# Kernel optimization log

Hardware: AMD Instinct MI355X
Metric: run time of the kernel (lower is better)

The kernel has to match this reference:

```python
import jax, jax.numpy as jnp
import numpy as np

K = 20
BN_EPS = 1e-5
NEG_SLOPE = 0.2


def knn_idx(x, k):
    # x: [B, C, N]; returns indices of k nearest neighbors per point: [B, N, k]
    sq = jnp.sum(x * x, axis=1)                      # [B, N]
    inner = jnp.einsum('bcn,bcm->bnm', x, x)         # [B, N, N]
    dist = sq[:, :, None] + sq[:, None, :] - 2.0 * inner  # squared distances
    _, idx = jax.lax.top_k(-dist, k)                 # smallest distances
    return idx


def get_graph_feature(x, k):
    # x: [B, C, N] -> [B, 2C, N, k]
    idx = knn_idx(x, k)                               # [B, N, k]
    gather = lambda xb, ib: xb[:, ib]                 # [C,N] x [N,k] -> [C,N,k]
    feature = jax.vmap(gather)(x, idx)                # [B, C, N, k]
    xk = jnp.broadcast_to(x[:, :, :, None], feature.shape)
    return jnp.concatenate([feature - xk, xk], axis=1)  # [B, 2C, N, k]


def setup_inputs() -> dict:
    key = jax.random.key(0)
    k1, k2 = jax.random.split(key)
    B, C, N = 8, 64, 4096
    x = jax.random.normal(k1, (B, C, N), dtype=jnp.float32)
    W = jax.random.normal(k2, (64, 2 * C), dtype=jnp.float32) * (1.0 / np.sqrt(2 * C))
    gamma = jnp.ones((64,), dtype=jnp.float32)
    beta = jnp.zeros((64,), dtype=jnp.float32)
    return {"x": x, "W": W, "gamma": gamma, "beta": beta}


def reference(x, W, gamma, beta):
    g = get_graph_feature(x, K)                       # [B, 2C, N, k]
    y = jnp.einsum('oc,bcnk->bonk', W, g)             # 1x1 conv, no bias
    # BatchNorm2d (training-mode batch statistics) over (B, N, k) per channel
    mean = jnp.mean(y, axis=(0, 2, 3), keepdims=True)
    var = jnp.var(y, axis=(0, 2, 3), keepdims=True)
    y = (y - mean) * jax.lax.rsqrt(var + BN_EPS)
    y = y * gamma[None, :, None, None] + beta[None, :, None, None]
    # LeakyReLU(0.2)
    y = jnp.where(y >= 0, y, NEG_SLOPE * y)
    # max over neighbors
    return jnp.max(y, axis=-1)                        # [B, out, N]
```

## Files before the change

kernel.cpp:

```cpp
#include <hip/hip_runtime.h>
#include <hip/hip_bf16.h>
#include <float.h>

#define BATCH 8
#define CDIM 64
#define NPTS 4096
#define KNN 20
#define KSEL 32
#define BUFCAP 128
#define BN_EPS 1e-5f
#define NEG_SLOPE 0.2f

typedef __attribute__((ext_vector_type(8))) short short8;
typedef __attribute__((ext_vector_type(4))) float float4v;
typedef unsigned short ushort;
typedef unsigned int uint;
typedef unsigned long long ull;

__device__ __forceinline__ ushort f2bf(float f) {
    uint u = __float_as_uint(f);
    u += 0x7FFF + ((u >> 16) & 1);
    return (ushort)(u >> 16);
}
__device__ __forceinline__ int mbcnt64(ull m) {
    int c = __builtin_amdgcn_mbcnt_lo((uint)m, 0);
    return __builtin_amdgcn_mbcnt_hi((uint)(m >> 32), c);
}

__device__ __forceinline__ uint select33_truncate(uint* __restrict__ buf,
                                                  int& cnt, int lane) {
    uint e0 = 0xFFFFFFFFu, e1 = 0xFFFFFFFFu;
    if (lane < cnt) e0 = buf[lane];
    if (64 + lane < cnt) e1 = buf[64 + lane];
    uint p = 0;
    for (int bit = 31; bit >= 0; --bit) {
        uint t = p | (1u << bit);
        ull mA = __ballot(e0 < t);
        ull mB = __ballot(e1 < t);
        if (__popcll(mA) + __popcll(mB) < 33) p = t;
    }
    ull mA = __ballot(e0 < p);
    ull mB = __ballot(e1 < p);
    int pA = __popcll(mA);
    int r0 = mbcnt64(mA);
    int r1 = pA + mbcnt64(mB);
    if (e0 < p) buf[r0] = e0;
    if (e1 < p) buf[r1] = e1;
    cnt = pA + __popcll(mB);
    return p;
}

__device__ __forceinline__ void scan_append(float dwv, float base, int idx,
                                            uint& tau, int& cnt,
                                            uint* __restrict__ buf, int lane) {
    float dval = fmaxf(fmaf(-2.f, dwv, base), 0.f);
    uint key = (__float_as_uint(dval) & 0xFFFFF000u) | (uint)idx;
    ull mask = __ballot(key < tau);
    if (mask) {
        int c = __popcll(mask);
        if (cnt + c > BUFCAP) {
            tau = select33_truncate(buf, cnt, lane);
            mask = __ballot(key < tau);
            c = __popcll(mask);
        }
        if (c) {
            int rank = mbcnt64(mask);
            if (key < tau) buf[cnt + rank] = key;
            cnt += c;
        }
    }
}


__global__ void __launch_bounds__(256) k_ppz(
        const float* __restrict__ x, const float* __restrict__ W,
        float* __restrict__ xt, ushort* __restrict__ xh,
        float* __restrict__ sq,
        float* __restrict__ pt, float* __restrict__ zt) {
    __shared__ float xs[64][65];
    __shared__ float sqred[4][64];

    int b  = blockIdx.x & 7;
    int n0 = (blockIdx.x >> 3) << 6;
    int lane = threadIdx.x & 63;
    int w = threadIdx.x >> 6;
    int row = b * NPTS + n0 + lane;

    const float* xb = x + (size_t)b * CDIM * NPTS + (n0 + lane);
    float v[16]; ushort h[16];
    float accq = 0.f;
    #pragma unroll
    for (int j = 0; j < 16; ++j) {
        float tv = xb[((w << 4) + j) * NPTS];
        v[j] = tv;
        accq = fmaf(tv, tv, accq);
        h[j] = f2bf(tv);
        xs[lane][(w << 4) + j] = tv;
    }
    {
        float4* xtv = (float4*)(xt + ((size_t)row << 6) + (w << 4));
        #pragma unroll
        for (int q = 0; q < 4; ++q)
            xtv[q] = make_float4(v[q*4], v[q*4+1], v[q*4+2], v[q*4+3]);
        uint4* xhp = (uint4*)(xh + ((size_t)row << 6) + (w << 4));
        uint4 p0, p1;
        p0.x = (uint)h[0] | ((uint)h[1] << 16);
        p0.y = (uint)h[2] | ((uint)h[3] << 16);
        p0.z = (uint)h[4] | ((uint)h[5] << 16);
        p0.w = (uint)h[6] | ((uint)h[7] << 16);
        p1.x = (uint)h[8] | ((uint)h[9] << 16);
        p1.y = (uint)h[10] | ((uint)h[11] << 16);
        p1.z = (uint)h[12] | ((uint)h[13] << 16);
        p1.w = (uint)h[14] | ((uint)h[15] << 16);
        xhp[0] = p0; xhp[1] = p1;
    }
    sqred[w][lane] = accq;
    __syncthreads();
    if (w == 0)
        sq[row] = sqred[0][lane] + sqred[1][lane] +
                  sqred[2][lane] + sqred[3][lane];

    size_t rowoff = ((size_t)row) << 6;
    float acc1[16], acc2[16];
    #pragma unroll
    for (int i = 0; i < 16; ++i) { acc1[i] = 0.f; acc2[i] = 0.f; }
    #pragma unroll
    for (int cg = 0; cg < 4; ++cg) {
        float xv[16];
        #pragma unroll
        for (int j = 0; j < 16; ++j)
            xv[j] = xs[lane][(cg << 4) + j];
        #pragma unroll
        for (int oi = 0; oi < 16; ++oi) {
            int o = (w << 4) + oi;
            const float* wr = W + o * 128 + cg * 16;
            float a1 = acc1[oi], a2 = acc2[oi];
            #pragma unroll
            for (int j = 0; j < 16; ++j) {
                a1 = fmaf(wr[j],      xv[j], a1);
                a2 = fmaf(wr[64 + j], xv[j], a2);
            }
            acc1[oi] = a1; acc2[oi] = a2;
        }
    }
    float4* pv = (float4*)(pt + rowoff + (w << 4));
    float4* zv = (float4*)(zt + rowoff + (w << 4));
    #pragma unroll
    for (int q = 0; q < 4; ++q) {
        pv[q] = make_float4(acc1[q*4], acc1[q*4+1], acc1[q*4+2], acc1[q*4+3]);
        zv[q] = make_float4(acc2[q*4]   - acc1[q*4],
                            acc2[q*4+1] - acc1[q*4+1],
                            acc2[q*4+2] - acc1[q*4+2],
                            acc2[q*4+3] - acc1[q*4+3]);
    }
}

__global__ void __launch_bounds__(256, 8) k_knn(
        const ushort* __restrict__ xh,
        const float* __restrict__ sq, ushort* __restrict__ knn32) {
    __shared__ float dw[2][64][20];
    __shared__ uint rowbuf[16 * BUFCAP];

    int tid  = threadIdx.x;
    int t    = tid >> 6;
    int lane = tid & 63;
    int b    = blockIdx.x & 7;
    int r0   = (blockIdx.x >> 3) << 4;
    int col  = lane & 15;
    int quad = lane >> 4;

    size_t arow = ((size_t)(b * NPTS + r0 + col)) << 6;
    short8 ah0 = *(const short8*)(xh + arow + quad * 8);
    short8 ah1 = *(const short8*)(xh + arow + 32 + quad * 8);

    const ushort* xhb = xh + (((size_t)b * NPTS) << 6);
    const float* sqb = sq + b * NPTS;
    const ushort* fbase = xhb + (((size_t)((t << 4) + col)) << 6) + (quad << 3);

    uint tau[4];
    int cnt[4];
    float sqr[4];
    uint* wbuf = rowbuf + ((t << 2) * BUFCAP);
    #pragma unroll
    for (int r = 0; r < 4; ++r) {
        tau[r] = 0xFFFFFFFFu; cnt[r] = 0;
        sqr[r] = sqb[r0 + (t << 2) + r];
    }

    short8 fA0 = *(const short8*)fbase;
    short8 fA1 = *(const short8*)(fbase + 32);
    short8 fB0, fB1;
    float sv_cur = 0.f;
    float sv_nxt = sqb[lane];

    auto step = [&](int c, int q, short8& f0, short8& f1,
                    short8& nf0, short8& nf1) {
        if (c + 1 < 64) {
            const ushort* p = fbase + (((size_t)(c + 1)) << 12);
            nf0 = *(const short8*)p;
            nf1 = *(const short8*)(p + 32);
        }
        float sv_tmp = (c + 1 < 64) ? sqb[((c + 1) << 6) + lane] : 0.f;

        float4v acc = {0.f, 0.f, 0.f, 0.f};
        acc = __builtin_amdgcn_mfma_f32_16x16x32_bf16(ah0, f0, acc, 0, 0, 0);
        acc = __builtin_amdgcn_mfma_f32_16x16x32_bf16(ah1, f1, acc, 0, 0, 0);
        *(float4v*)&dw[q][(t << 4) + col][quad << 2] = acc;

        if (c > 0) {
            int m0 = (c - 1) << 6;
            float4v dv4 = *(const float4v*)&dw[q ^ 1][lane][t << 2];
            #pragma unroll
            for (int r = 0; r < 4; ++r) {
                scan_append(dv4[r], sv_cur + sqr[r], m0 + lane, tau[r], cnt[r],
                            wbuf + r * BUFCAP, lane);
            }
        }
        sv_cur = sv_nxt;
        sv_nxt = sv_tmp;

        __builtin_amdgcn_sched_barrier(0);
        asm volatile("s_waitcnt lgkmcnt(0)" ::: "memory");
        __builtin_amdgcn_s_barrier();
        __builtin_amdgcn_sched_barrier(0);
    };

    for (int c = 0; c < 64; c += 2) {
        step(c,     0, fA0, fA1, fB0, fB1);
        step(c + 1, 1, fB0, fB1, fA0, fA1);
    }

    {
        int m0 = 63 << 6;
        float4v dv4 = *(const float4v*)&dw[1][lane][t << 2];
        #pragma unroll
        for (int r = 0; r < 4; ++r) {
            scan_append(dv4[r], sv_cur + sqr[r], m0 + lane, tau[r], cnt[r],
                        wbuf + r * BUFCAP, lane);
        }
    }

    #pragma unroll
    for (int r = 0; r < 4; ++r) {
        select33_truncate(wbuf + r * BUFCAP, cnt[r], lane);
        if (lane < KSEL) {
            uint e = wbuf[r * BUFCAP + lane];
            knn32[(size_t)(b * NPTS + r0 + (t << 2) + r) * KSEL + lane] =
                (ushort)(e & 0xFFFu);
        }
    }
}

__global__ void __launch_bounds__(256) k_refine(
        const float* __restrict__ xt, const float* __restrict__ sq,
        const ushort* __restrict__ knn32, int* __restrict__ idx20) {
    int b    = blockIdx.x & 7;
    int j    = blockIdx.x >> 3;
    int lane = threadIdx.x & 63;
    int wv   = threadIdx.x >> 6;
    int half = lane >> 5;
    int sl   = lane & 31;
    int row  = (b << 12) + (j << 3) + (wv << 1) + half;
    int cand = knn32[(size_t)row * KSEL + sl];
    const float4* xc = (const float4*)(xt + ((size_t)((b << 12) + cand) << 6));
    const float4* xr = (const float4*)(xt + ((size_t)row << 6));
    float acc = 0.f;
    #pragma unroll
    for (int q = 0; q < 16; ++q) {
        float4 a = xr[q], c = xc[q];
        acc = fmaf(a.x, c.x, acc); acc = fmaf(a.y, c.y, acc);
        acc = fmaf(a.z, c.z, acc); acc = fmaf(a.w, c.w, acc);
    }
    float d = fmaf(-2.f, acc, sq[(b << 12) + cand]);
    int rank = 0;
    int base = half << 5;
    #pragma unroll
    for (int jj = 0; jj < KSEL; ++jj) {
        float dj = __shfl(d, base + jj);
        int   cj = __shfl(cand, base + jj);
        rank += ((dj < d) || (dj == d && cj < cand)) ? 1 : 0;
    }
    if (rank < KNN)
        idx20[(size_t)row * KNN + rank] = cand;
}

__global__ void k_stat(const float* __restrict__ pt, const float* __restrict__ zt,
                       const int* __restrict__ idxin,
                       float* __restrict__ S1, float* __restrict__ S2) {
    __shared__ float red1[4][64];
    __shared__ float red2[4][64];
    int b  = blockIdx.x & 7;
    int n0 = (blockIdx.x >> 3) << 6;
    int lane = threadIdx.x & 63;
    int w = threadIdx.x >> 6;
    float cs1 = 0.f, cs2 = 0.f;
    for (int i = 0; i < 16; ++i) {
        int n = n0 + (w << 4) + i;
        int base = b * NPTS + n;
        int ibase = __builtin_amdgcn_readfirstlane(base * KNN);
        const int* ip = idxin + ibase;
        float s1 = 0.f, s2 = 0.f;
        #pragma unroll
        for (int k = 0; k < KNN; ++k) {
            int colp = ip[k];
            float v = pt[(((size_t)(b * NPTS + colp)) << 6) + lane];
            s1 += v; s2 = fmaf(v, v, s2);
        }
        float z = zt[(((size_t)base) << 6) + lane];
        cs1 += s1 + (float)KNN * z;
        cs2 += s2 + 2.f * z * s1 + (float)KNN * z * z;
    }
    red1[w][lane] = cs1;
    red2[w][lane] = cs2;
    __syncthreads();
    if (threadIdx.x < 64) {
        float t1 = red1[0][lane] + red1[1][lane] + red1[2][lane] + red1[3][lane];
        float t2 = red2[0][lane] + red2[1][lane] + red2[2][lane] + red2[3][lane];
        atomicAdd(&S1[lane], t1);
        atomicAdd(&S2[lane], t2);
    }
}

__global__ void __launch_bounds__(256) k_fin(
        const float* __restrict__ pt, const float* __restrict__ zt,
        const int* __restrict__ idxin,
        const float* __restrict__ S1, const float* __restrict__ S2,
        const float* __restrict__ gamma, const float* __restrict__ beta,
        float* __restrict__ out) {
    __shared__ float sy[64][65];
    int b  = blockIdx.x & 7;
    int n0 = (blockIdx.x >> 3) << 6;
    int lane = threadIdx.x & 63;
    int w = threadIdx.x >> 6;

    const float inv_cnt = 1.0f / ((float)BATCH * NPTS * KNN);
    float s1 = S1[lane], s2 = S2[lane];
    float mean = s1 * inv_cnt;
    float var = fmaf(-mean, mean, s2 * inv_cnt);
    float rs = rsqrtf(var + BN_EPS);
    float sc = gamma[lane] * rs;
    float sh = beta[lane] - mean * sc;
    bool useMax = (sc >= 0.f);

    for (int i = 0; i < 16; ++i) {
        int nl = (w << 4) + i;
        int base = b * NPTS + n0 + nl;
        int ibase = __builtin_amdgcn_readfirstlane(base * KNN);
        const int* ip = idxin + ibase;
        float mx = -FLT_MAX, mn = FLT_MAX;
        #pragma unroll
        for (int k = 0; k < KNN; ++k) {
            int colp = ip[k];
            float v = pt[(((size_t)(b * NPTS + colp)) << 6) + lane];
            mx = fmaxf(mx, v); mn = fminf(mn, v);
        }
        float z = zt[(((size_t)base) << 6) + lane];
        float tv = (useMax ? mx : mn) + z;
        float y = fmaf(tv, sc, sh);
        y = (y >= 0.f) ? y : NEG_SLOPE * y;
        sy[nl][lane] = y;
    }
    __syncthreads();
    #pragma unroll
    for (int i = 0; i < 16; ++i) {
        int o = (i << 2) + w;
        out[((size_t)(b * 64 + o)) * NPTS + n0 + lane] = sy[lane][o];
    }
}

extern "C" void kernel_launch(void* const* d_in, const int* in_sizes, int n_in,
                              void* d_out, int out_size, void* d_ws, size_t ws_size,
                              hipStream_t stream) {
    const float* x     = (const float*)d_in[0];
    const float* W     = (const float*)d_in[1];
    const float* gamma = (const float*)d_in[2];
    const float* beta  = (const float*)d_in[3];
    float* out = (float*)d_out;

    float* ws = (float*)d_ws;
    const size_t SECT = (size_t)BATCH * NPTS * 64;
    float*  xt    = ws;
    float*  pt    = ws + SECT;
    float*  zt    = ws + 2 * SECT;
    float*  sq    = ws + 3 * SECT;
    float*  S1    = ws + 3 * SECT + 32768;
    float*  S2    = S1 + 64;
    int*    idx20 = (int*)(S1 + 128);
    float*  uA    = ws + 3 * SECT + 32768 + 128 + 655360;
    ushort* xh    = (ushort*)uA;
    ushort* knn32 = (ushort*)(uA + SECT / 2);

    hipMemsetAsync(S1, 0, 128 * sizeof(float), stream);
    k_ppz   <<<dim3(BATCH * (NPTS / 64)), dim3(256), 0, stream>>>(x, W, xt, xh, sq, pt, zt);
    k_knn   <<<dim3(BATCH * (NPTS / 16)), dim3(256), 0, stream>>>(xh, sq, knn32);
    k_refine<<<dim3((BATCH * NPTS) / 8), dim3(256), 0, stream>>>(xt, sq, knn32, idx20);
    k_stat  <<<dim3(BATCH * (NPTS / 64)), dim3(256), 0, stream>>>(pt, zt, idx20, S1, S2);
    k_fin   <<<dim3(BATCH * (NPTS / 64)), dim3(256), 0, stream>>>(pt, zt, idx20, S1, S2, gamma, beta, out);
}
```

Before: 330.8 us.

## Fuse kNN refine with stats gather and cache fp16 max/min for final pass

Merges the refine and BN-statistics kernels so the top-20 indices stay in shared memory and are never written to global memory. In the same gather pass it computes per-channel max and min plus the center term, packs them as two fp16 values and stores them, so the final kernel reads one word per output instead of re-gathering 20 neighbors. The S1/S2 zeroing moves into the first kernel, which removes the memset launch. The fp16 storage of max/min lowers precision of the pre-normalization values and may exceed tolerance. Zeroing S1 in block 0 of k_ppz is ordered before the atomics because they happen in a later kernel on the same stream.

Result: slower. 339.1 us (+2.5%).

```diff
diff --git a/kernel.cpp b/kernel.cpp
--- a/kernel.cpp
+++ b/kernel.cpp
@@ -1,5 +1,6 @@
 #include <hip/hip_runtime.h>
 #include <hip/hip_bf16.h>
+#include <hip/hip_fp16.h>
 #include <float.h>
 
 #define BATCH 8
@@ -76,9 +77,13 @@
         const float* __restrict__ x, const float* __restrict__ W,
         float* __restrict__ xt, ushort* __restrict__ xh,
         float* __restrict__ sq,
-        float* __restrict__ pt, float* __restrict__ zt) {
+        float* __restrict__ pt, float* __restrict__ zt,
+        float* __restrict__ S1) {
     __shared__ float xs[64][65];
     __shared__ float sqred[4][64];
+
+    if (blockIdx.x == 0 && threadIdx.x < 128)
+        S1[threadIdx.x] = 0.f;
 
     int b  = blockIdx.x & 7;
     int n0 = (blockIdx.x >> 3) << 6;
@@ -251,67 +256,72 @@
     }
 }
 
-__global__ void __launch_bounds__(256) k_refine(
+__global__ void __launch_bounds__(256) k_refgather(
         const float* __restrict__ xt, const float* __restrict__ sq,
-        const ushort* __restrict__ knn32, int* __restrict__ idx20) {
+        const ushort* __restrict__ knn32,
+        const float* __restrict__ pt, const float* __restrict__ zt,
+        float* __restrict__ S1, float* __restrict__ S2,
+        uint* __restrict__ tmm) {
+    __shared__ int tops[16][20];
+    __shared__ float red1[4][64];
+    __shared__ float red2[4][64];
+
     int b    = blockIdx.x & 7;
-    int j    = blockIdx.x >> 3;
+    int n0   = (blockIdx.x >> 3) << 4;
     int lane = threadIdx.x & 63;
     int wv   = threadIdx.x >> 6;
     int half = lane >> 5;
     int sl   = lane & 31;
-    int row  = (b << 12) + (j << 3) + (wv << 1) + half;
-    int cand = knn32[(size_t)row * KSEL + sl];
-    const float4* xc = (const float4*)(xt + ((size_t)((b << 12) + cand) << 6));
-    const float4* xr = (const float4*)(xt + ((size_t)row << 6));
-    float acc = 0.f;
-    #pragma unroll
-    for (int q = 0; q < 16; ++q) {
-        float4 a = xr[q], c = xc[q];
-        acc = fmaf(a.x, c.x, acc); acc = fmaf(a.y, c.y, acc);
-        acc = fmaf(a.z, c.z, acc); acc = fmaf(a.w, c.w, acc);
-    }
-    float d = fmaf(-2.f, acc, sq[(b << 12) + cand]);
-    int rank = 0;
-    int base = half << 5;
-    #pragma unroll
-    for (int jj = 0; jj < KSEL; ++jj) {
-        float dj = __shfl(d, base + jj);
-        int   cj = __shfl(cand, base + jj);
-        rank += ((dj < d) || (dj == d && cj < cand)) ? 1 : 0;
-    }
-    if (rank < KNN)
-        idx20[(size_t)row * KNN + rank] = cand;
-}
-
-__global__ void k_stat(const float* __restrict__ pt, const float* __restrict__ zt,
-                       const int* __restrict__ idxin,
-                       float* __restrict__ S1, float* __restrict__ S2) {
-    __shared__ float red1[4][64];
-    __shared__ float red2[4][64];
-    int b  = blockIdx.x & 7;
-    int n0 = (blockIdx.x >> 3) << 6;
-    int lane = threadIdx.x & 63;
-    int w = threadIdx.x >> 6;
+    const float* sqb = sq + b * NPTS;
+
+    #pragma unroll 1
+    for (int pr = 0; pr < 2; ++pr) {
+        int rloc = (wv << 2) + (pr << 1) + half;
+        int row  = b * NPTS + n0 + rloc;
+        int cand = knn32[(size_t)row * KSEL + sl];
+        const float4* xc = (const float4*)(xt + ((size_t)(b * NPTS + cand) << 6));
+        const float4* xr = (const float4*)(xt + ((size_t)row << 6));
+        float acc = 0.f;
+        #pragma unroll
+        for (int q = 0; q < 16; ++q) {
+            float4 a = xr[q], c4 = xc[q];
+            acc = fmaf(a.x, c4.x, acc); acc = fmaf(a.y, c4.y, acc);
+            acc = fmaf(a.z, c4.z, acc); acc = fmaf(a.w, c4.w, acc);
+        }
+        float d = fmaf(-2.f, acc, sqb[cand]);
+        int rank = 0;
+        int base = half << 5;
+        #pragma unroll
+        for (int j = 0; j < KSEL; ++j) {
+            float dj = __shfl(d, base + j);
+            int   cj = __shfl(cand, base + j);
+            rank += ((dj < d) || (dj == d && cj < cand)) ? 1 : 0;
+        }
+        if (rank < KNN) tops[rloc][rank] = cand;
+    }
+
     float cs1 = 0.f, cs2 = 0.f;
-    for (int i = 0; i < 16; ++i) {
-        int n = n0 + (w << 4) + i;
-        int base = b * NPTS + n;
-        int ibase = __builtin_amdgcn_readfirstlane(base * KNN);
-        const int* ip = idxin + ibase;
-        float s1 = 0.f, s2 = 0.f;
+    #pragma unroll 1
+    for (int i = 0; i < 4; ++i) {
+        int rloc = (wv << 2) + i;
+        int base = b * NPTS + n0 + rloc;
+        float s1r = 0.f, s2r = 0.f, mx = -FLT_MAX, mn = FLT_MAX;
         #pragma unroll
         for (int k = 0; k < KNN; ++k) {
-            int colp = ip[k];
+            int colp = tops[rloc][k];
             float v = pt[(((size_t)(b * NPTS + colp)) << 6) + lane];
-            s1 += v; s2 = fmaf(v, v, s2);
+            s1r += v; s2r = fmaf(v, v, s2r);
+            mx = fmaxf(mx, v); mn = fminf(mn, v);
         }
         float z = zt[(((size_t)base) << 6) + lane];
-        cs1 += s1 + (float)KNN * z;
-        cs2 += s2 + 2.f * z * s1 + (float)KNN * z * z;
-    }
-    red1[w][lane] = cs1;
-    red2[w][lane] = cs2;
+        uint pk = (uint)__half_as_ushort(__float2half(mx + z)) |
+                  ((uint)__half_as_ushort(__float2half(mn + z)) << 16);
+        tmm[(((size_t)base) << 6) + lane] = pk;
+        cs1 += s1r + (float)KNN * z;
+        cs2 += s2r + 2.f * z * s1r + (float)KNN * z * z;
+    }
+    red1[wv][lane] = cs1;
+    red2[wv][lane] = cs2;
     __syncthreads();
     if (threadIdx.x < 64) {
         float t1 = red1[0][lane] + red1[1][lane] + red1[2][lane] + red1[3][lane];
@@ -321,9 +331,8 @@
     }
 }
 
-__global__ void __launch_bounds__(256) k_fin(
-        const float* __restrict__ pt, const float* __restrict__ zt,
-        const int* __restrict__ idxin,
+__global__ void __launch_bounds__(256) k_fin2(
+        const uint* __restrict__ tmm,
         const float* __restrict__ S1, const float* __restrict__ S2,
         const float* __restrict__ gamma, const float* __restrict__ beta,
         float* __restrict__ out) {
@@ -342,20 +351,14 @@
     float sh = beta[lane] - mean * sc;
     bool useMax = (sc >= 0.f);
 
+    #pragma unroll
     for (int i = 0; i < 16; ++i) {
         int nl = (w << 4) + i;
         int base = b * NPTS + n0 + nl;
-        int ibase = __builtin_amdgcn_readfirstlane(base * KNN);
-        const int* ip = idxin + ibase;
-        float mx = -FLT_MAX, mn = FLT_MAX;
-        #pragma unroll
-        for (int k = 0; k < KNN; ++k) {
-            int colp = ip[k];
-            float v = pt[(((size_t)(b * NPTS + colp)) << 6) + lane];
-            mx = fmaxf(mx, v); mn = fminf(mn, v);
-        }
-        float z = zt[(((size_t)base) << 6) + lane];
-        float tv = (useMax ? mx : mn) + z;
+        uint pk = tmm[(((size_t)base) << 6) + lane];
+        float mxz = __half2float(__ushort_as_half((ushort)(pk & 0xFFFFu)));
+        float mnz = __half2float(__ushort_as_half((ushort)(pk >> 16)));
+        float tv = useMax ? mxz : mnz;
         float y = fmaf(tv, sc, sh);
         y = (y >= 0.f) ? y : NEG_SLOPE * y;
         sy[nl][lane] = y;
@@ -385,15 +388,12 @@
     float*  sq    = ws + 3 * SECT;
     float*  S1    = ws + 3 * SECT + 32768;
     float*  S2    = S1 + 64;
-    int*    idx20 = (int*)(S1 + 128);
-    float*  uA    = ws + 3 * SECT + 32768 + 128 + 655360;
-    ushort* xh    = (ushort*)uA;
-    ushort* knn32 = (ushort*)(uA + SECT / 2);
-
-    hipMemsetAsync(S1, 0, 128 * sizeof(float), stream);
-    k_ppz   <<<dim3(BATCH * (NPTS / 64)), dim3(256), 0, stream>>>(x, W, xt, xh, sq, pt, zt);
-    k_knn   <<<dim3(BATCH * (NPTS / 16)), dim3(256), 0, stream>>>(xh, sq, knn32);
-    k_refine<<<dim3((BATCH * NPTS) / 8), dim3(256), 0, stream>>>(xt, sq, knn32, idx20);
-    k_stat  <<<dim3(BATCH * (NPTS / 64)), dim3(256), 0, stream>>>(pt, zt, idx20, S1, S2);
-    k_fin   <<<dim3(BATCH * (NPTS / 64)), dim3(256), 0, stream>>>(pt, zt, idx20, S1, S2, gamma, beta, out);
-}
+    uint*   tmm   = (uint*)(S1 + 128);
+    ushort* xh    = (ushort*)(S1 + 128 + SECT);
+    ushort* knn32 = xh + SECT;
+
+    k_ppz      <<<dim3(BATCH * (NPTS / 64)), dim3(256), 0, stream>>>(x, W, xt, xh, sq, pt, zt, S1);
+    k_knn      <<<dim3(BATCH * (NPTS / 16)), dim3(256), 0, stream>>>(xh, sq, knn32);
+    k_refgather<<<dim3(BATCH * (NPTS / 16)), dim3(256), 0, stream>>>(xt, sq, knn32, pt, zt, S1, S2, tmm);
+    k_fin2     <<<dim3(BATCH * (NPTS / 64)), dim3(256), 0, stream>>>(tmm, S1, S2, gamma, beta, out);
+}
```
